# Kernel tuning notes

Hardware: AMD Instinct MI355X
Metric: run time of the kernel (lower is better)

Reference implementation:

```python
import jax, jax.numpy as jnp
import numpy as np

LEVELS = 8
DB2 = [0.4829629131445341, 0.8365163037378079, 0.22414386804185735, -0.12940952255092145]


def make_wavelet(h):
    # g = flip(h); g[1::2] *= -1  (torch compute_wavelet)
    g = jnp.flip(h, -1)
    sign = jnp.where(jnp.arange(g.shape[-1]) % 2 == 0, 1.0, -1.0).astype(g.dtype)
    return g * sign


def circ_conv(x, f, tr=False):
    # FFT-based circular convolution, output length == input length (NORM='backward').
    L = x.shape[-1]
    F = jnp.fft.rfft(f, n=L)
    if tr:
        F = jnp.conj(F)  # circular correlation for the synthesis side
    return jnp.fft.irfft(jnp.fft.rfft(x, n=L) * F, n=L)


def despawn_forward(x, scaling):
    levels = scaling.shape[0]
    L = x.shape[1]
    D = 2 ** int(np.ceil(np.log2(L)))
    pl = (D - L) // 2
    pr = int(np.ceil((D - L) / 2))
    x = jnp.pad(x, ((0, 0), (pl, pr)), mode='edge')  # ReplicationPad1d

    # Analysis: per-level circular filter + dyadic downsample
    approx = x
    details_list = []
    for lev in range(levels):
        h = scaling[lev]
        g = make_wavelet(h)
        d = circ_conv(approx, g)[:, ::2]
        approx = circ_conv(approx, h)[:, ::2]
        details_list.append(d)
    coeffs = details_list + [approx]

    # Synthesis: zero-insert upsample + circular correlation (no thresholding,
    # matching the original forward which never applies HardThreshold)
    rec = approx
    for lev in reversed(range(levels)):
        h = scaling[lev]
        g = make_wavelet(h)
        d = details_list[lev]
        n, m = d.shape
        ud = jnp.zeros((n, 2 * m), d.dtype).at[:, ::2].set(d)
        ua = jnp.zeros((n, 2 * m), rec.dtype).at[:, ::2].set(rec)
        rec = circ_conv(ud, g, tr=True) + circ_conv(ua, h, tr=True)

    return rec[:, pl:L + pr], jnp.concatenate(coeffs, axis=-1)


def setup_inputs() -> dict:
    key = jax.random.key(0)
    k1, _ = jax.random.split(key)
    x = jax.random.normal(k1, (2048, 8192), dtype=jnp.float32)
    scaling = jnp.tile(jnp.asarray(DB2, dtype=jnp.float32), (LEVELS, 1))  # (levels, 4)
    return {"x": x, "scaling": scaling}


def reference(x, scaling):
    return despawn_forward(x, scaling)
```

## Files before the change

kernel.cpp:

```cpp
#include <hip/hip_runtime.h>

#define COLS   8192
#define LEVELS 8
#define TPB    512

__device__ __forceinline__ void bar_lds() {
    asm volatile("s_waitcnt lgkmcnt(0)" ::: "memory");
    __builtin_amdgcn_sched_barrier(0);
    __builtin_amdgcn_s_barrier();
    __builtin_amdgcn_sched_barrier(0);
}

__global__ __launch_bounds__(TPB) void despawn_kernel(
    const float* __restrict__ x, const float* __restrict__ scaling,
    float* __restrict__ out, int rows)
{
    __shared__ __align__(16) float B[COLS / 2];
    __shared__ __align__(16) float C[COLS / 4];
    __shared__ __align__(16) float D[COLS / 4];
    __shared__ float filt[LEVELS * 4];

    const int row = blockIdx.x;
    const int tid = threadIdx.x;

    if (tid < LEVELS * 4) filt[tid] = scaling[tid];
    bar_lds();

    const float* __restrict__ xg       = x + (size_t)row * COLS;
    float* __restrict__       out_rec  = out + (size_t)row * COLS;
    float* __restrict__       out_coef = out + (size_t)rows * COLS + (size_t)row * COLS;

    {
        const float h0 = filt[0], h1 = filt[1], h2 = filt[2], h3 = filt[3];
        const float g0 = h3, g1 = -h2, g2 = h1, g3 = -h0;
        const float4* __restrict__ xg4 = reinterpret_cast<const float4*>(xg);
        const int q8 = COLS / 8, qm = COLS / 4 - 1;
        for (int i = tid; i < q8; i += TPB) {
            const float4 va = xg4[(2 * i - 1) & qm];
            const float4 vb = xg4[2 * i];
            const float4 vc = xg4[2 * i + 1];
            float4 dv, av;
            dv.x = g0*vb.x + g1*va.w + g2*va.z + g3*va.y;
            av.x = h0*vb.x + h1*va.w + h2*va.z + h3*va.y;
            dv.y = g0*vb.z + g1*vb.y + g2*vb.x + g3*va.w;
            av.y = h0*vb.z + h1*vb.y + h2*vb.x + h3*va.w;
            dv.z = g0*vc.x + g1*vb.w + g2*vb.z + g3*vb.y;
            av.z = h0*vc.x + h1*vb.w + h2*vb.z + h3*vb.y;
            dv.w = g0*vc.z + g1*vc.y + g2*vc.x + g3*vb.w;
            av.w = h0*vc.z + h1*vc.y + h2*vc.x + h3*vb.w;
            reinterpret_cast<float4*>(out_coef)[i] = dv;
            reinterpret_cast<float4*>(B)[i]        = av;
        }
        bar_lds();
    }

    int n = COLS / 2, coff = COLS / 2, dOff = 0;
    float* cur = B;
    float* nxt = C;
    for (int lev = 1; lev <= 3; ++lev) {
        const float h0 = filt[4*lev+0], h1 = filt[4*lev+1],
                    h2 = filt[4*lev+2], h3 = filt[4*lev+3];
        const float g0 = h3, g1 = -h2, g2 = h1, g3 = -h0;
        const int half = n >> 1, qq = half >> 2, qm = (n >> 2) - 1;
        const float4* c4 = reinterpret_cast<const float4*>(cur);
        float4* o4 = reinterpret_cast<float4*>(out_coef + coff);
        float4* n4 = reinterpret_cast<float4*>(nxt);
        float4* D4 = reinterpret_cast<float4*>(D + dOff);
        const bool toD = (lev >= 2);
        for (int p = tid; p < qq; p += TPB) {
            const float4 va = c4[(2 * p - 1) & qm];
            const float4 vb = c4[2 * p];
            const float4 vc = c4[2 * p + 1];
            float4 dv, av;
            dv.x = g0*vb.x + g1*va.w + g2*va.z + g3*va.y;
            av.x = h0*vb.x + h1*va.w + h2*va.z + h3*va.y;
            dv.y = g0*vb.z + g1*vb.y + g2*vb.x + g3*va.w;
            av.y = h0*vb.z + h1*vb.y + h2*vb.x + h3*va.w;
            dv.z = g0*vc.x + g1*vb.w + g2*vb.z + g3*vb.y;
            av.z = h0*vc.x + h1*vb.w + h2*vb.z + h3*vb.y;
            dv.w = g0*vc.z + g1*vc.y + g2*vc.x + g3*vb.w;
            av.w = h0*vc.z + h1*vc.y + h2*vc.x + h3*vb.w;
            o4[p] = dv;
            n4[p] = av;
            if (toD) D4[p] = dv;
        }
        bar_lds();
        coff += half;
        if (toD) dOff += half;
        n = half;
        float* t = cur; cur = nxt; nxt = t;
    }

    if (tid < 64) {
        float* acur = C;
        float* anxt = B;
        int nn = 512, coffW = 7680, dW = 1536;
        for (int lev = 4; lev <= 7; ++lev) {
            const float h0 = filt[4*lev+0], h1 = filt[4*lev+1],
                        h2 = filt[4*lev+2], h3 = filt[4*lev+3];
            const float g0 = h3, g1 = -h2, g2 = h1, g3 = -h0;
            const int half = nn >> 1, mask = nn - 1;
            for (int i = tid; i < half; i += 64) {
                const int b = 2 * i;
                const float x0 = acur[b];
                const float x1 = acur[(b - 1) & mask];
                const float x2 = acur[(b - 2) & mask];
                const float x3 = acur[(b - 3) & mask];
                const float d = g0*x0 + g1*x1 + g2*x2 + g3*x3;
                const float a = h0*x0 + h1*x1 + h2*x2 + h3*x3;
                D[dW + i] = d;
                out_coef[coffW + i] = d;
                if (lev == 7) { D[2016 + i] = a; out_coef[8160 + i] = a; }
                else          anxt[i] = a;
            }
            __builtin_amdgcn_wave_barrier();
            coffW += half; dW += half; nn = half;
            float* t = acur; acur = anxt; anxt = t;
        }
        int mS = 32, dS = 1984;
        const float* aprevW = D + 2016;
        for (int lev = 7; lev >= 4; --lev) {
            const float h0 = filt[4*lev+0], h1 = filt[4*lev+1],
                        h2 = filt[4*lev+2], h3 = filt[4*lev+3];
            const float g0 = h3, g1 = -h2, g2 = h1, g3 = -h0;
            const int mm = mS - 1;
            float* recW = (lev & 1) ? B : C;
            for (int j = tid; j < mS; j += 64) {
                const float dj  = D[dS + j];
                const float dj1 = D[dS + ((j + 1) & mm)];
                const float dj2 = D[dS + ((j + 2) & mm)];
                const float aj  = aprevW[j];
                const float aj1 = aprevW[(j + 1) & mm];
                const float aj2 = aprevW[(j + 2) & mm];
                recW[2*j]     = g0*dj  + g2*dj1 + h0*aj  + h2*aj1;
                recW[2*j + 1] = g1*dj1 + g3*dj2 + h1*aj1 + h3*aj2;
            }
            __builtin_amdgcn_wave_barrier();
            aprevW = recW; mS <<= 1; dS -= mS;
        }
    }
    __syncthreads();

#define SYNTH_BODY(d2)                                                        \
    for (int p = tid; p < mp; p += TPB) {                                     \
        const float2 dv0 = (d2)[p];                                           \
        const float2 dv1 = (d2)[(p + 1) & mm];                                \
        const float2 av0 = a2[p];                                             \
        const float2 av1 = a2[(p + 1) & mm];                                  \
        const float r0 = g0*dv0.x + g2*dv0.y + h0*av0.x + h2*av0.y;           \
        const float r1 = g1*dv0.y + g3*dv1.x + h1*av0.y + h3*av1.x;           \
        const float r2 = g0*dv0.y + g2*dv1.x + h0*av0.y + h2*av1.x;           \
        const float r3 = g1*dv1.x + g3*dv1.y + h1*av1.x + h3*av1.y;           \
        const float4 rv = make_float4(r0, r1, r2, r3);                        \
        if (last) reinterpret_cast<float4*>(out_rec)[p] = rv;                 \
        else      reinterpret_cast<float4*>(rec)[p]     = rv;                 \
    }

    const float* aprev = C;
    int m = 512;
    for (int lev = 3; lev >= 0; --lev) {
        const float h0 = filt[4*lev+0], h1 = filt[4*lev+1],
                    h2 = filt[4*lev+2], h3 = filt[4*lev+3];
        const float g0 = h3, g1 = -h2, g2 = h1, g3 = -h0;
        const int mp = m >> 1, mm = mp - 1;
        const float2* a2 = reinterpret_cast<const float2*>(aprev);
        float* rec = (lev & 1) ? B : C;
        const bool last = (lev == 0);
        if (lev >= 2) {
            const float2* dL = reinterpret_cast<const float2*>(D + ((lev == 3) ? 1024 : 0));
            SYNTH_BODY(dL)
        } else {
            const float2* __restrict__ dG =
                reinterpret_cast<const float2*>(out_coef + ((lev == 1) ? 4096 : 0));
            SYNTH_BODY(dG)
        }
        if (lev) bar_lds();
        aprev = rec; m <<= 1;
    }
#undef SYNTH_BODY
}

extern "C" void kernel_launch(void* const* d_in, const int* in_sizes, int n_in,
                              void* d_out, int out_size, void* d_ws, size_t ws_size,
                              hipStream_t stream) {
    const float* x       = (const float*)d_in[0];
    const float* scaling = (const float*)d_in[1];
    float* out           = (float*)d_out;
    const int rows = in_sizes[0] / COLS;
    despawn_kernel<<<rows, TPB, 0, stream>>>(x, scaling, out, rows);
}
```

Baseline: 42.76 us.

## Split fused wavelet kernel into separate analysis and synthesis launches

Splits the single per-row kernel into an analysis kernel and a synthesis kernel. The analysis kernel finishes levels 4-7 and the coarse synthesis with one wave, after the other waves exit early, and parks the level-4 approximation in the output buffer. The synthesis kernel reads the detail coefficients and that intermediate back from global memory to do levels 3-0. The intent is that idle waves no longer wait on the single-wave tail section and that the smaller LDS footprint allows higher occupancy. The cost is a second launch and extra global traffic for the re-read coefficients.

```diff
diff --git a/kernel.cpp b/kernel.cpp
--- a/kernel.cpp
+++ b/kernel.cpp
@@ -1,8 +1,7 @@
 #include <hip/hip_runtime.h>
 
-#define COLS   8192
-#define LEVELS 8
-#define TPB    512
+#define COLS 8192
+#define TPB  512
 
 __device__ __forceinline__ void bar_lds() {
     asm volatile("s_waitcnt lgkmcnt(0)" ::: "memory");
@@ -11,19 +10,17 @@
     __builtin_amdgcn_sched_barrier(0);
 }
 
-__global__ __launch_bounds__(TPB) void despawn_kernel(
+__global__ __launch_bounds__(TPB) void despawn_analysis(
     const float* __restrict__ x, const float* __restrict__ scaling,
     float* __restrict__ out, int rows)
 {
-    __shared__ __align__(16) float B[COLS / 2];
-    __shared__ __align__(16) float C[COLS / 4];
-    __shared__ __align__(16) float D[COLS / 4];
-    __shared__ float filt[LEVELS * 4];
+    __shared__ __align__(16) float LA[4096];
+    __shared__ __align__(16) float LB[2048];
+    __shared__ float filt[32];
 
     const int row = blockIdx.x;
     const int tid = threadIdx.x;
-
-    if (tid < LEVELS * 4) filt[tid] = scaling[tid];
+    if (tid < 32) filt[tid] = scaling[tid];
     bar_lds();
 
     const float* __restrict__ xg       = x + (size_t)row * COLS;
@@ -49,133 +46,217 @@
             dv.w = g0*vc.z + g1*vc.y + g2*vc.x + g3*vb.w;
             av.w = h0*vc.z + h1*vc.y + h2*vc.x + h3*vb.w;
             reinterpret_cast<float4*>(out_coef)[i] = dv;
-            reinterpret_cast<float4*>(B)[i]        = av;
-        }
-        bar_lds();
-    }
-
-    int n = COLS / 2, coff = COLS / 2, dOff = 0;
-    float* cur = B;
-    float* nxt = C;
-    for (int lev = 1; lev <= 3; ++lev) {
-        const float h0 = filt[4*lev+0], h1 = filt[4*lev+1],
-                    h2 = filt[4*lev+2], h3 = filt[4*lev+3];
-        const float g0 = h3, g1 = -h2, g2 = h1, g3 = -h0;
-        const int half = n >> 1, qq = half >> 2, qm = (n >> 2) - 1;
-        const float4* c4 = reinterpret_cast<const float4*>(cur);
-        float4* o4 = reinterpret_cast<float4*>(out_coef + coff);
-        float4* n4 = reinterpret_cast<float4*>(nxt);
-        float4* D4 = reinterpret_cast<float4*>(D + dOff);
-        const bool toD = (lev >= 2);
-        for (int p = tid; p < qq; p += TPB) {
-            const float4 va = c4[(2 * p - 1) & qm];
-            const float4 vb = c4[2 * p];
-            const float4 vc = c4[2 * p + 1];
-            float4 dv, av;
-            dv.x = g0*vb.x + g1*va.w + g2*va.z + g3*va.y;
-            av.x = h0*vb.x + h1*va.w + h2*va.z + h3*va.y;
-            dv.y = g0*vb.z + g1*vb.y + g2*vb.x + g3*va.w;
-            av.y = h0*vb.z + h1*vb.y + h2*vb.x + h3*va.w;
-            dv.z = g0*vc.x + g1*vb.w + g2*vb.z + g3*vb.y;
-            av.z = h0*vc.x + h1*vb.w + h2*vb.z + h3*vb.y;
-            dv.w = g0*vc.z + g1*vc.y + g2*vc.x + g3*vb.w;
-            av.w = h0*vc.z + h1*vc.y + h2*vc.x + h3*vb.w;
-            o4[p] = dv;
-            n4[p] = av;
-            if (toD) D4[p] = dv;
-        }
-        bar_lds();
-        coff += half;
-        if (toD) dOff += half;
-        n = half;
-        float* t = cur; cur = nxt; nxt = t;
-    }
-
-    if (tid < 64) {
-        float* acur = C;
-        float* anxt = B;
-        int nn = 512, coffW = 7680, dW = 1536;
-        for (int lev = 4; lev <= 7; ++lev) {
+            reinterpret_cast<float4*>(LA)[i]       = av;
+        }
+        bar_lds();
+    }
+
+    {
+        int n = 4096, coff = 4096;
+        float* cur = LA;
+        float* nxt = LB;
+        for (int lev = 1; lev <= 3; ++lev) {
             const float h0 = filt[4*lev+0], h1 = filt[4*lev+1],
                         h2 = filt[4*lev+2], h3 = filt[4*lev+3];
             const float g0 = h3, g1 = -h2, g2 = h1, g3 = -h0;
-            const int half = nn >> 1, mask = nn - 1;
-            for (int i = tid; i < half; i += 64) {
-                const int b = 2 * i;
-                const float x0 = acur[b];
-                const float x1 = acur[(b - 1) & mask];
-                const float x2 = acur[(b - 2) & mask];
-                const float x3 = acur[(b - 3) & mask];
-                const float d = g0*x0 + g1*x1 + g2*x2 + g3*x3;
-                const float a = h0*x0 + h1*x1 + h2*x2 + h3*x3;
-                D[dW + i] = d;
-                out_coef[coffW + i] = d;
-                if (lev == 7) { D[2016 + i] = a; out_coef[8160 + i] = a; }
-                else          anxt[i] = a;
+            const int half = n >> 1, qq = half >> 2, qm = (n >> 2) - 1;
+            const float4* c4 = reinterpret_cast<const float4*>(cur);
+            float4* o4 = reinterpret_cast<float4*>(out_coef + coff);
+            float4* n4 = reinterpret_cast<float4*>(nxt);
+            for (int p = tid; p < qq; p += TPB) {
+                const float4 va = c4[(2 * p - 1) & qm];
+                const float4 vb = c4[2 * p];
+                const float4 vc = c4[2 * p + 1];
+                float4 dv, av;
+                dv.x = g0*vb.x + g1*va.w + g2*va.z + g3*va.y;
+                av.x = h0*vb.x + h1*va.w + h2*va.z + h3*va.y;
+                dv.y = g0*vb.z + g1*vb.y + g2*vb.x + g3*va.w;
+                av.y = h0*vb.z + h1*vb.y + h2*vb.x + h3*va.w;
+                dv.z = g0*vc.x + g1*vb.w + g2*vb.z + g3*vb.y;
+                av.z = h0*vc.x + h1*vb.w + h2*vb.z + h3*vb.y;
+                dv.w = g0*vc.z + g1*vc.y + g2*vc.x + g3*vb.w;
+                av.w = h0*vc.z + h1*vc.y + h2*vc.x + h3*vb.w;
+                o4[p] = dv;
+                n4[p] = av;
             }
-            __builtin_amdgcn_wave_barrier();
-            coffW += half; dW += half; nn = half;
-            float* t = acur; acur = anxt; anxt = t;
-        }
-        int mS = 32, dS = 1984;
-        const float* aprevW = D + 2016;
-        for (int lev = 7; lev >= 4; --lev) {
-            const float h0 = filt[4*lev+0], h1 = filt[4*lev+1],
-                        h2 = filt[4*lev+2], h3 = filt[4*lev+3];
-            const float g0 = h3, g1 = -h2, g2 = h1, g3 = -h0;
-            const int mm = mS - 1;
-            float* recW = (lev & 1) ? B : C;
-            for (int j = tid; j < mS; j += 64) {
-                const float dj  = D[dS + j];
-                const float dj1 = D[dS + ((j + 1) & mm)];
-                const float dj2 = D[dS + ((j + 2) & mm)];
-                const float aj  = aprevW[j];
-                const float aj1 = aprevW[(j + 1) & mm];
-                const float aj2 = aprevW[(j + 2) & mm];
-                recW[2*j]     = g0*dj  + g2*dj1 + h0*aj  + h2*aj1;
-                recW[2*j + 1] = g1*dj1 + g3*dj2 + h1*aj1 + h3*aj2;
-            }
-            __builtin_amdgcn_wave_barrier();
-            aprevW = recW; mS <<= 1; dS -= mS;
-        }
-    }
-    __syncthreads();
-
-#define SYNTH_BODY(d2)                                                        \
+            bar_lds();
+            coff += half;
+            n = half;
+            float* t = cur; cur = nxt; nxt = t;
+        }
+    }
+
+    if (tid >= 64) return;
+
+    float* P = LA;
+    float* Q = LA + 512;
+    float* Y = LA + 1024;
+    const int lane = tid;
+
+    {
+        const float h0=filt[16],h1=filt[17],h2=filt[18],h3=filt[19];
+        const float g0=h3,g1=-h2,g2=h1,g3=-h0;
+        for (int i = lane; i < 256; i += 64) {
+            const int b = 2*i;
+            const float x0=LB[b], x1=LB[(b-1)&511], x2=LB[(b-2)&511], x3=LB[(b-3)&511];
+            const float d = g0*x0+g1*x1+g2*x2+g3*x3;
+            Y[i] = d; out_coef[7680+i] = d;
+            P[i] = h0*x0+h1*x1+h2*x2+h3*x3;
+        }
+        __builtin_amdgcn_wave_barrier();
+    }
+    {
+        const float h0=filt[20],h1=filt[21],h2=filt[22],h3=filt[23];
+        const float g0=h3,g1=-h2,g2=h1,g3=-h0;
+        for (int i = lane; i < 128; i += 64) {
+            const int b = 2*i;
+            const float x0=P[b], x1=P[(b-1)&255], x2=P[(b-2)&255], x3=P[(b-3)&255];
+            const float d = g0*x0+g1*x1+g2*x2+g3*x3;
+            Y[256+i] = d; out_coef[7936+i] = d;
+            Q[i] = h0*x0+h1*x1+h2*x2+h3*x3;
+        }
+        __builtin_amdgcn_wave_barrier();
+    }
+    {
+        const float h0=filt[24],h1=filt[25],h2=filt[26],h3=filt[27];
+        const float g0=h3,g1=-h2,g2=h1,g3=-h0;
+        if (lane < 64) {
+            const int i = lane, b = 2*i;
+            const float x0=Q[b], x1=Q[(b-1)&127], x2=Q[(b-2)&127], x3=Q[(b-3)&127];
+            const float d = g0*x0+g1*x1+g2*x2+g3*x3;
+            Y[384+i] = d; out_coef[8064+i] = d;
+            P[i] = h0*x0+h1*x1+h2*x2+h3*x3;
+        }
+        __builtin_amdgcn_wave_barrier();
+    }
+    {
+        const float h0=filt[28],h1=filt[29],h2=filt[30],h3=filt[31];
+        const float g0=h3,g1=-h2,g2=h1,g3=-h0;
+        if (lane < 32) {
+            const int i = lane, b = 2*i;
+            const float x0=P[b], x1=P[(b-1)&63], x2=P[(b-2)&63], x3=P[(b-3)&63];
+            const float d = g0*x0+g1*x1+g2*x2+g3*x3;
+            const float a = h0*x0+h1*x1+h2*x2+h3*x3;
+            Y[448+i] = d; out_coef[8128+i] = d;
+            Y[480+i] = a; out_coef[8160+i] = a;
+        }
+        __builtin_amdgcn_wave_barrier();
+    }
+    {
+        const float h0=filt[28],h1=filt[29],h2=filt[30],h3=filt[31];
+        const float g0=h3,g1=-h2,g2=h1,g3=-h0;
+        if (lane < 32) {
+            const int j = lane;
+            const float dj=Y[448+j], dj1=Y[448+((j+1)&31)], dj2=Y[448+((j+2)&31)];
+            const float aj=Y[480+j], aj1=Y[480+((j+1)&31)], aj2=Y[480+((j+2)&31)];
+            Q[2*j]   = g0*dj  + g2*dj1 + h0*aj  + h2*aj1;
+            Q[2*j+1] = g1*dj1 + g3*dj2 + h1*aj1 + h3*aj2;
+        }
+        __builtin_amdgcn_wave_barrier();
+    }
+    {
+        const float h0=filt[24],h1=filt[25],h2=filt[26],h3=filt[27];
+        const float g0=h3,g1=-h2,g2=h1,g3=-h0;
+        if (lane < 64) {
+            const int j = lane;
+            const float dj=Y[384+j], dj1=Y[384+((j+1)&63)], dj2=Y[384+((j+2)&63)];
+            const float aj=Q[j], aj1=Q[(j+1)&63], aj2=Q[(j+2)&63];
+            P[2*j]   = g0*dj  + g2*dj1 + h0*aj  + h2*aj1;
+            P[2*j+1] = g1*dj1 + g3*dj2 + h1*aj1 + h3*aj2;
+        }
+        __builtin_amdgcn_wave_barrier();
+    }
+    {
+        const float h0=filt[20],h1=filt[21],h2=filt[22],h3=filt[23];
+        const float g0=h3,g1=-h2,g2=h1,g3=-h0;
+        for (int j = lane; j < 128; j += 64) {
+            const float dj=Y[256+j], dj1=Y[256+((j+1)&127)], dj2=Y[256+((j+2)&127)];
+            const float aj=P[j], aj1=P[(j+1)&127], aj2=P[(j+2)&127];
+            Q[2*j]   = g0*dj  + g2*dj1 + h0*aj  + h2*aj1;
+            Q[2*j+1] = g1*dj1 + g3*dj2 + h1*aj1 + h3*aj2;
+        }
+        __builtin_amdgcn_wave_barrier();
+    }
+    {
+        const float h0=filt[16],h1=filt[17],h2=filt[18],h3=filt[19];
+        const float g0=h3,g1=-h2,g2=h1,g3=-h0;
+        float2* __restrict__ st = reinterpret_cast<float2*>(out_rec + 512);
+        for (int j = lane; j < 256; j += 64) {
+            const float dj=Y[j], dj1=Y[(j+1)&255], dj2=Y[(j+2)&255];
+            const float aj=Q[j], aj1=Q[(j+1)&255], aj2=Q[(j+2)&255];
+            const float r0 = g0*dj  + g2*dj1 + h0*aj  + h2*aj1;
+            const float r1 = g1*dj1 + g3*dj2 + h1*aj1 + h3*aj2;
+            st[j] = make_float2(r0, r1);
+        }
+    }
+}
+
+__global__ __launch_bounds__(TPB) void despawn_synth(
+    const float* __restrict__ scaling, float* __restrict__ out, int rows)
+{
+    __shared__ __align__(16) float LA[4096];
+    __shared__ __align__(16) float LB[4096];
+    __shared__ float filt[32];
+
+    const int row = blockIdx.x;
+    const int tid = threadIdx.x;
+    if (tid < 32) filt[tid] = scaling[tid];
+    bar_lds();
+
+    float* __restrict__       out_rec  = out + (size_t)row * COLS;
+    const float* __restrict__ out_coef = out + (size_t)rows * COLS + (size_t)row * COLS;
+
+#define SYNTH_BODY(d2, a2, dst4, toG)                                         \
     for (int p = tid; p < mp; p += TPB) {                                     \
         const float2 dv0 = (d2)[p];                                           \
         const float2 dv1 = (d2)[(p + 1) & mm];                                \
-        const float2 av0 = a2[p];                                             \
-        const float2 av1 = a2[(p + 1) & mm];                                  \
+        const float2 av0 = (a2)[p];                                           \
+        const float2 av1 = (a2)[(p + 1) & mm];                                \
         const float r0 = g0*dv0.x + g2*dv0.y + h0*av0.x + h2*av0.y;           \
         const float r1 = g1*dv0.y + g3*dv1.x + h1*av0.y + h3*av1.x;           \
         const float r2 = g0*dv0.y + g2*dv1.x + h0*av0.y + h2*av1.x;           \
         const float r3 = g1*dv1.x + g3*dv1.y + h1*av1.x + h3*av1.y;           \
-        const float4 rv = make_float4(r0, r1, r2, r3);                        \
-        if (last) reinterpret_cast<float4*>(out_rec)[p] = rv;                 \
-        else      reinterpret_cast<float4*>(rec)[p]     = rv;                 \
-    }
-
-    const float* aprev = C;
-    int m = 512;
-    for (int lev = 3; lev >= 0; --lev) {
-        const float h0 = filt[4*lev+0], h1 = filt[4*lev+1],
-                    h2 = filt[4*lev+2], h3 = filt[4*lev+3];
-        const float g0 = h3, g1 = -h2, g2 = h1, g3 = -h0;
-        const int mp = m >> 1, mm = mp - 1;
-        const float2* a2 = reinterpret_cast<const float2*>(aprev);
-        float* rec = (lev & 1) ? B : C;
-        const bool last = (lev == 0);
-        if (lev >= 2) {
-            const float2* dL = reinterpret_cast<const float2*>(D + ((lev == 3) ? 1024 : 0));
-            SYNTH_BODY(dL)
-        } else {
-            const float2* __restrict__ dG =
-                reinterpret_cast<const float2*>(out_coef + ((lev == 1) ? 4096 : 0));
-            SYNTH_BODY(dG)
-        }
-        if (lev) bar_lds();
-        aprev = rec; m <<= 1;
+        (dst4)[p] = make_float4(r0, r1, r2, r3);                              \
+    }
+
+    {
+        const float h0=filt[12],h1=filt[13],h2=filt[14],h3=filt[15];
+        const float g0=h3,g1=-h2,g2=h1,g3=-h0;
+        const int mp = 256, mm = 255;
+        const float2* __restrict__ d2 = reinterpret_cast<const float2*>(out_coef + 7168);
+        const float2* __restrict__ a2 = reinterpret_cast<const float2*>(out_rec + 512);
+        float4* dst4 = reinterpret_cast<float4*>(LB);
+        SYNTH_BODY(d2, a2, dst4, false)
+        bar_lds();
+    }
+    {
+        const float h0=filt[8],h1=filt[9],h2=filt[10],h3=filt[11];
+        const float g0=h3,g1=-h2,g2=h1,g3=-h0;
+        const int mp = 512, mm = 511;
+        const float2* __restrict__ d2 = reinterpret_cast<const float2*>(out_coef + 6144);
+        const float2* a2 = reinterpret_cast<const float2*>(LB);
+        float4* dst4 = reinterpret_cast<float4*>(LA);
+        SYNTH_BODY(d2, a2, dst4, false)
+        bar_lds();
+    }
+    {
+        const float h0=filt[4],h1=filt[5],h2=filt[6],h3=filt[7];
+        const float g0=h3,g1=-h2,g2=h1,g3=-h0;
+        const int mp = 1024, mm = 1023;
+        const float2* __restrict__ d2 = reinterpret_cast<const float2*>(out_coef + 4096);
+        const float2* a2 = reinterpret_cast<const float2*>(LA);
+        float4* dst4 = reinterpret_cast<float4*>(LB);
+        SYNTH_BODY(d2, a2, dst4, false)
+        bar_lds();
+    }
+    {
+        const float h0=filt[0],h1=filt[1],h2=filt[2],h3=filt[3];
+        const float g0=h3,g1=-h2,g2=h1,g3=-h0;
+        const int mp = 2048, mm = 2047;
+        const float2* __restrict__ d2 = reinterpret_cast<const float2*>(out_coef);
+        const float2* a2 = reinterpret_cast<const float2*>(LB);
+        float4* __restrict__ dst4 = reinterpret_cast<float4*>(out_rec);
+        SYNTH_BODY(d2, a2, dst4, true)
     }
 #undef SYNTH_BODY
 }
@@ -187,5 +268,6 @@
     const float* scaling = (const float*)d_in[1];
     float* out           = (float*)d_out;
     const int rows = in_sizes[0] / COLS;
-    despawn_kernel<<<rows, TPB, 0, stream>>>(x, scaling, out, rows);
-}
+    despawn_analysis<<<rows, TPB, 0, stream>>>(x, scaling, out, rows);
+    despawn_synth<<<rows, TPB, 0, stream>>>(scaling, out, rows);
+}
```

Result: slower. 48.39 us (+13.1%).

## Replace single-wave tail and barriered synthesis with register/shuffle per-wave pipeline

Applied to the files above, without the earlier changes.

Every wave now redundantly computes analysis levels 4-7 and synthesis levels 7-4 in registers using cross-lane shuffles, instead of one wave working through LDS while the other waves wait. Synthesis levels 3-0 are then computed per wave from registers, with halo values recomputed locally. This removes the block-wide barriers between those levels. Filters are read directly from global memory rather than staged in LDS. The cost is duplicated arithmetic and higher register pressure, plus fragile index logic at the boundaries.

```diff
diff --git a/kernel.cpp b/kernel.cpp
--- a/kernel.cpp
+++ b/kernel.cpp
@@ -1,8 +1,7 @@
 #include <hip/hip_runtime.h>
 
-#define COLS   8192
-#define LEVELS 8
-#define TPB    512
+#define COLS 8192
+#define TPB  512
 
 __device__ __forceinline__ void bar_lds() {
     asm volatile("s_waitcnt lgkmcnt(0)" ::: "memory");
@@ -10,28 +9,65 @@
     __builtin_amdgcn_s_barrier();
     __builtin_amdgcn_sched_barrier(0);
 }
+__device__ __forceinline__ void wait_lds() {
+    asm volatile("s_waitcnt lgkmcnt(0)" ::: "memory");
+    __builtin_amdgcn_sched_barrier(0);
+}
+
+#define ANA_LEVEL(CIN, ain, aout, dout, F0, F1, F2, F3)                       \
+    {                                                                         \
+        const int _src = (l - 1) & 63;                                        \
+        const float _m1 = __shfl(ain[(CIN)-1], _src);                         \
+        const float _m2 = __shfl(ain[(CIN)-2], _src);                         \
+        const float _m3 = __shfl(ain[(CIN)-3], _src);                         \
+        dout[0] = (F3)*ain[0] - (F2)*_m1 + (F1)*_m2 - (F0)*_m3;               \
+        aout[0] = (F0)*ain[0] + (F1)*_m1 + (F2)*_m2 + (F3)*_m3;               \
+        dout[1] = (F3)*ain[2] - (F2)*ain[1] + (F1)*ain[0] - (F0)*_m1;         \
+        aout[1] = (F0)*ain[2] + (F1)*ain[1] + (F2)*ain[0] + (F3)*_m1;         \
+        _Pragma("unroll")                                                     \
+        for (int _j = 2; _j < (CIN)/2; ++_j) {                                \
+            dout[_j] = (F3)*ain[2*_j] - (F2)*ain[2*_j-1] + (F1)*ain[2*_j-2] - (F0)*ain[2*_j-3]; \
+            aout[_j] = (F0)*ain[2*_j] + (F1)*ain[2*_j-1] + (F2)*ain[2*_j-2] + (F3)*ain[2*_j-3]; \
+        }                                                                     \
+    }
+
+#define SYN_LEVEL(CD, din, ain, rout, F0, F1, F2, F3)                         \
+    {                                                                         \
+        const int _src = (l + 1) & 63;                                        \
+        const float _d0 = __shfl(din[0], _src);                               \
+        const float _d1 = __shfl(din[1], _src);                               \
+        const float _a0 = __shfl(ain[0], _src);                               \
+        const float _a1 = __shfl(ain[1], _src);                               \
+        _Pragma("unroll")                                                     \
+        for (int _j = 0; _j < (CD); ++_j) {                                   \
+            const float dj  = din[_j];                                        \
+            const float dj1 = (_j+1 < (CD)) ? din[_j+1] : _d0;                \
+            const float dj2 = (_j+2 < (CD)) ? din[_j+2] : ((_j+1 < (CD)) ? _d0 : _d1); \
+            const float aj  = ain[_j];                                        \
+            const float aj1 = (_j+1 < (CD)) ? ain[_j+1] : _a0;                \
+            const float aj2 = (_j+2 < (CD)) ? ain[_j+2] : ((_j+1 < (CD)) ? _a0 : _a1); \
+            rout[2*_j]   = (F3)*dj + (F1)*dj1 + (F0)*aj + (F2)*aj1;           \
+            rout[2*_j+1] = -(F2)*dj1 - (F0)*dj2 + (F1)*aj1 + (F3)*aj2;        \
+        }                                                                     \
+    }
 
 __global__ __launch_bounds__(TPB) void despawn_kernel(
     const float* __restrict__ x, const float* __restrict__ scaling,
     float* __restrict__ out, int rows)
 {
-    __shared__ __align__(16) float B[COLS / 2];
-    __shared__ __align__(16) float C[COLS / 4];
-    __shared__ __align__(16) float D[COLS / 4];
-    __shared__ float filt[LEVELS * 4];
+    __shared__ __align__(16) float B[4096];
+    __shared__ __align__(16) float C[2048];
+    __shared__ __align__(16) float D[1536];
 
     const int row = blockIdx.x;
     const int tid = threadIdx.x;
-
-    if (tid < LEVELS * 4) filt[tid] = scaling[tid];
-    bar_lds();
 
     const float* __restrict__ xg       = x + (size_t)row * COLS;
     float* __restrict__       out_rec  = out + (size_t)row * COLS;
     float* __restrict__       out_coef = out + (size_t)rows * COLS + (size_t)row * COLS;
 
     {
-        const float h0 = filt[0], h1 = filt[1], h2 = filt[2], h3 = filt[3];
+        const float h0 = scaling[0], h1 = scaling[1], h2 = scaling[2], h3 = scaling[3];
         const float g0 = h3, g1 = -h2, g2 = h1, g3 = -h0;
         const float4* __restrict__ xg4 = reinterpret_cast<const float4*>(xg);
         const int q8 = COLS / 8, qm = COLS / 4 - 1;
@@ -54,130 +90,219 @@
         bar_lds();
     }
 
-    int n = COLS / 2, coff = COLS / 2, dOff = 0;
-    float* cur = B;
-    float* nxt = C;
-    for (int lev = 1; lev <= 3; ++lev) {
-        const float h0 = filt[4*lev+0], h1 = filt[4*lev+1],
-                    h2 = filt[4*lev+2], h3 = filt[4*lev+3];
-        const float g0 = h3, g1 = -h2, g2 = h1, g3 = -h0;
-        const int half = n >> 1, qq = half >> 2, qm = (n >> 2) - 1;
-        const float4* c4 = reinterpret_cast<const float4*>(cur);
-        float4* o4 = reinterpret_cast<float4*>(out_coef + coff);
-        float4* n4 = reinterpret_cast<float4*>(nxt);
-        float4* D4 = reinterpret_cast<float4*>(D + dOff);
-        const bool toD = (lev >= 2);
-        for (int p = tid; p < qq; p += TPB) {
-            const float4 va = c4[(2 * p - 1) & qm];
-            const float4 vb = c4[2 * p];
-            const float4 vc = c4[2 * p + 1];
-            float4 dv, av;
-            dv.x = g0*vb.x + g1*va.w + g2*va.z + g3*va.y;
-            av.x = h0*vb.x + h1*va.w + h2*va.z + h3*va.y;
-            dv.y = g0*vb.z + g1*vb.y + g2*vb.x + g3*va.w;
-            av.y = h0*vb.z + h1*vb.y + h2*vb.x + h3*va.w;
-            dv.z = g0*vc.x + g1*vb.w + g2*vb.z + g3*vb.y;
-            av.z = h0*vc.x + h1*vb.w + h2*vb.z + h3*vb.y;
-            dv.w = g0*vc.z + g1*vc.y + g2*vc.x + g3*vb.w;
-            av.w = h0*vc.z + h1*vc.y + h2*vc.x + h3*vb.w;
-            o4[p] = dv;
-            n4[p] = av;
-            if (toD) D4[p] = dv;
-        }
-        bar_lds();
-        coff += half;
-        if (toD) dOff += half;
-        n = half;
-        float* t = cur; cur = nxt; nxt = t;
-    }
-
-    if (tid < 64) {
-        float* acur = C;
-        float* anxt = B;
-        int nn = 512, coffW = 7680, dW = 1536;
-        for (int lev = 4; lev <= 7; ++lev) {
-            const float h0 = filt[4*lev+0], h1 = filt[4*lev+1],
-                        h2 = filt[4*lev+2], h3 = filt[4*lev+3];
+    {
+        int n = COLS / 2, coff = COLS / 2, dOff = 0;
+        float* cur = B;
+        float* nxt = C;
+        for (int lev = 1; lev <= 3; ++lev) {
+            const float h0 = scaling[4*lev+0], h1 = scaling[4*lev+1],
+                        h2 = scaling[4*lev+2], h3 = scaling[4*lev+3];
             const float g0 = h3, g1 = -h2, g2 = h1, g3 = -h0;
-            const int half = nn >> 1, mask = nn - 1;
-            for (int i = tid; i < half; i += 64) {
-                const int b = 2 * i;
-                const float x0 = acur[b];
-                const float x1 = acur[(b - 1) & mask];
-                const float x2 = acur[(b - 2) & mask];
-                const float x3 = acur[(b - 3) & mask];
-                const float d = g0*x0 + g1*x1 + g2*x2 + g3*x3;
-                const float a = h0*x0 + h1*x1 + h2*x2 + h3*x3;
-                D[dW + i] = d;
-                out_coef[coffW + i] = d;
-                if (lev == 7) { D[2016 + i] = a; out_coef[8160 + i] = a; }
-                else          anxt[i] = a;
+            const int half = n >> 1, qq = half >> 2, qm = (n >> 2) - 1;
+            const float4* c4 = reinterpret_cast<const float4*>(cur);
+            float4* o4 = reinterpret_cast<float4*>(out_coef + coff);
+            float4* n4 = reinterpret_cast<float4*>(nxt);
+            float4* D4 = reinterpret_cast<float4*>(D + dOff);
+            const bool toD = (lev >= 2);
+            for (int p = tid; p < qq; p += TPB) {
+                const float4 va = c4[(2 * p - 1) & qm];
+                const float4 vb = c4[2 * p];
+                const float4 vc = c4[2 * p + 1];
+                float4 dv, av;
+                dv.x = g0*vb.x + g1*va.w + g2*va.z + g3*va.y;
+                av.x = h0*vb.x + h1*va.w + h2*va.z + h3*va.y;
+                dv.y = g0*vb.z + g1*vb.y + g2*vb.x + g3*va.w;
+                av.y = h0*vb.z + h1*vb.y + h2*vb.x + h3*va.w;
+                dv.z = g0*vc.x + g1*vb.w + g2*vb.z + g3*vb.y;
+                av.z = h0*vc.x + h1*vb.w + h2*vb.z + h3*vb.y;
+                dv.w = g0*vc.z + g1*vc.y + g2*vc.x + g3*vb.w;
+                av.w = h0*vc.z + h1*vc.y + h2*vc.x + h3*vb.w;
+                o4[p] = dv;
+                n4[p] = av;
+                if (toD) D4[p] = dv;
             }
-            __builtin_amdgcn_wave_barrier();
-            coffW += half; dW += half; nn = half;
-            float* t = acur; acur = anxt; anxt = t;
-        }
-        int mS = 32, dS = 1984;
-        const float* aprevW = D + 2016;
-        for (int lev = 7; lev >= 4; --lev) {
-            const float h0 = filt[4*lev+0], h1 = filt[4*lev+1],
-                        h2 = filt[4*lev+2], h3 = filt[4*lev+3];
-            const float g0 = h3, g1 = -h2, g2 = h1, g3 = -h0;
-            const int mm = mS - 1;
-            float* recW = (lev & 1) ? B : C;
-            for (int j = tid; j < mS; j += 64) {
-                const float dj  = D[dS + j];
-                const float dj1 = D[dS + ((j + 1) & mm)];
-                const float dj2 = D[dS + ((j + 2) & mm)];
-                const float aj  = aprevW[j];
-                const float aj1 = aprevW[(j + 1) & mm];
-                const float aj2 = aprevW[(j + 2) & mm];
-                recW[2*j]     = g0*dj  + g2*dj1 + h0*aj  + h2*aj1;
-                recW[2*j + 1] = g1*dj1 + g3*dj2 + h1*aj1 + h3*aj2;
-            }
-            __builtin_amdgcn_wave_barrier();
-            aprevW = recW; mS <<= 1; dS -= mS;
-        }
-    }
-    __syncthreads();
-
-#define SYNTH_BODY(d2)                                                        \
-    for (int p = tid; p < mp; p += TPB) {                                     \
-        const float2 dv0 = (d2)[p];                                           \
-        const float2 dv1 = (d2)[(p + 1) & mm];                                \
-        const float2 av0 = a2[p];                                             \
-        const float2 av1 = a2[(p + 1) & mm];                                  \
-        const float r0 = g0*dv0.x + g2*dv0.y + h0*av0.x + h2*av0.y;           \
-        const float r1 = g1*dv0.y + g3*dv1.x + h1*av0.y + h3*av1.x;           \
-        const float r2 = g0*dv0.y + g2*dv1.x + h0*av0.y + h2*av1.x;           \
-        const float r3 = g1*dv1.x + g3*dv1.y + h1*av1.x + h3*av1.y;           \
-        const float4 rv = make_float4(r0, r1, r2, r3);                        \
-        if (last) reinterpret_cast<float4*>(out_rec)[p] = rv;                 \
-        else      reinterpret_cast<float4*>(rec)[p]     = rv;                 \
-    }
-
-    const float* aprev = C;
-    int m = 512;
-    for (int lev = 3; lev >= 0; --lev) {
-        const float h0 = filt[4*lev+0], h1 = filt[4*lev+1],
-                    h2 = filt[4*lev+2], h3 = filt[4*lev+3];
-        const float g0 = h3, g1 = -h2, g2 = h1, g3 = -h0;
-        const int mp = m >> 1, mm = mp - 1;
-        const float2* a2 = reinterpret_cast<const float2*>(aprev);
-        float* rec = (lev & 1) ? B : C;
-        const bool last = (lev == 0);
-        if (lev >= 2) {
-            const float2* dL = reinterpret_cast<const float2*>(D + ((lev == 3) ? 1024 : 0));
-            SYNTH_BODY(dL)
-        } else {
-            const float2* __restrict__ dG =
-                reinterpret_cast<const float2*>(out_coef + ((lev == 1) ? 4096 : 0));
-            SYNTH_BODY(dG)
-        }
-        if (lev) bar_lds();
-        aprev = rec; m <<= 1;
-    }
-#undef SYNTH_BODY
+            if (lev == 3) __syncthreads();
+            else          bar_lds();
+            coff += half;
+            if (toD) dOff += half;
+            n = half;
+            float* t = cur; cur = nxt; nxt = t;
+        }
+    }
+
+    const int w = tid >> 6;
+    const int l = tid & 63;
+
+    float a3r[8];
+    {
+        const float4 v0 = reinterpret_cast<const float4*>(C)[2*l];
+        const float4 v1 = reinterpret_cast<const float4*>(C)[2*l+1];
+        a3r[0]=v0.x; a3r[1]=v0.y; a3r[2]=v0.z; a3r[3]=v0.w;
+        a3r[4]=v1.x; a3r[5]=v1.y; a3r[6]=v1.z; a3r[7]=v1.w;
+    }
+    float a4r[4], d4r[4];
+    ANA_LEVEL(8, a3r, a4r, d4r, scaling[16], scaling[17], scaling[18], scaling[19]);
+    float a5r[2], d5r[2];
+    ANA_LEVEL(4, a4r, a5r, d5r, scaling[20], scaling[21], scaling[22], scaling[23]);
+    float a6r, d6r;
+    {
+        const float F0=scaling[24],F1=scaling[25],F2=scaling[26],F3=scaling[27];
+        const int s1 = (l-1)&63, s2 = (l-2)&63;
+        const float x0 = a5r[0];
+        const float x1 = __shfl(a5r[1], s1);
+        const float x2 = __shfl(a5r[0], s1);
+        const float x3 = __shfl(a5r[1], s2);
+        d6r = F3*x0 - F2*x1 + F1*x2 - F0*x3;
+        a6r = F0*x0 + F1*x1 + F2*x2 + F3*x3;
+    }
+    float d7r, apr;
+    {
+        const float F0=scaling[28],F1=scaling[29],F2=scaling[30],F3=scaling[31];
+        const int i2 = 2*l;
+        const float x0 = __shfl(a6r, i2 & 63);
+        const float x1 = __shfl(a6r, (i2-1)&63);
+        const float x2 = __shfl(a6r, (i2-2)&63);
+        const float x3 = __shfl(a6r, (i2-3)&63);
+        d7r = F3*x0 - F2*x1 + F1*x2 - F0*x3;
+        apr = F0*x0 + F1*x1 + F2*x2 + F3*x3;
+    }
+    if (w == 0) {
+        reinterpret_cast<float4*>(out_coef + 7680)[l] = make_float4(d4r[0],d4r[1],d4r[2],d4r[3]);
+        reinterpret_cast<float2*>(out_coef + 7936)[l] = make_float2(d5r[0],d5r[1]);
+        out_coef[8064 + l] = d6r;
+        if (l < 32) { out_coef[8128 + l] = d7r; out_coef[8160 + l] = apr; }
+    }
+    float rec7;
+    {
+        const float F0=scaling[28],F1=scaling[29],F2=scaling[30],F3=scaling[31];
+        const float dj = d7r, dj1 = __shfl(d7r,(l+1)&31), dj2 = __shfl(d7r,(l+2)&31);
+        const float aj = apr, aj1 = __shfl(apr,(l+1)&31), aj2 = __shfl(apr,(l+2)&31);
+        const float r0 = F3*dj + F1*dj1 + F0*aj + F2*aj1;
+        const float r1 = -F2*dj1 - F0*dj2 + F1*aj1 + F3*aj2;
+        const float e0 = __shfl(r0, l>>1);
+        const float e1 = __shfl(r1, l>>1);
+        rec7 = (l & 1) ? e1 : e0;
+    }
+    float rec6[2];
+    {
+        const float F0=scaling[24],F1=scaling[25],F2=scaling[26],F3=scaling[27];
+        const float dj = d6r, dj1 = __shfl(d6r,(l+1)&63), dj2 = __shfl(d6r,(l+2)&63);
+        const float aj = rec7, aj1 = __shfl(rec7,(l+1)&63), aj2 = __shfl(rec7,(l+2)&63);
+        rec6[0] = F3*dj + F1*dj1 + F0*aj + F2*aj1;
+        rec6[1] = -F2*dj1 - F0*dj2 + F1*aj1 + F3*aj2;
+    }
+    float rec5[4];
+    SYN_LEVEL(2, d5r, rec6, rec5, scaling[20], scaling[21], scaling[22], scaling[23]);
+    float rec4r[8];
+    SYN_LEVEL(4, d4r, rec5, rec4r, scaling[16], scaling[17], scaling[18], scaling[19]);
+    reinterpret_cast<float4*>(C + 512)[2*l]   = make_float4(rec4r[0],rec4r[1],rec4r[2],rec4r[3]);
+    reinterpret_cast<float4*>(C + 512)[2*l+1] = make_float4(rec4r[4],rec4r[5],rec4r[6],rec4r[7]);
+    wait_lds();
+
+    float rec3[2], r3h[4];
+    {
+        const float F0=scaling[12],F1=scaling[13],F2=scaling[14],F3=scaling[15];
+        const int j = 64*w + l;
+        const float a0v = C[512 + (j & 511)];
+        const float a1v = C[512 + ((j+1) & 511)];
+        const float a2v = C[512 + ((j+2) & 511)];
+        const float e0  = D[1024 + (j & 511)];
+        const float e1  = D[1024 + ((j+1) & 511)];
+        const float e2  = D[1024 + ((j+2) & 511)];
+        rec3[0] = F3*e0 + F1*e1 + F0*a0v + F2*a1v;
+        rec3[1] = -F2*e1 - F0*e2 + F1*a1v + F3*a2v;
+        #pragma unroll
+        for (int q = 0; q < 2; ++q) {
+            const int jh = 64*(w+1) + q;
+            const float A0 = C[512 + (jh & 511)];
+            const float A1 = C[512 + ((jh+1) & 511)];
+            const float A2 = C[512 + ((jh+2) & 511)];
+            const float E0 = D[1024 + (jh & 511)];
+            const float E1 = D[1024 + ((jh+1) & 511)];
+            const float E2 = D[1024 + ((jh+2) & 511)];
+            r3h[2*q]   = F3*E0 + F1*E1 + F0*A0 + F2*A1;
+            r3h[2*q+1] = -F2*E1 - F0*E2 + F1*A1 + F3*A2;
+        }
+    }
+    float rec2[4], r2h[3];
+    {
+        const float F0=scaling[8],F1=scaling[9],F2=scaling[10],F3=scaling[11];
+        const int lp1 = (l+1)&63;
+        const float n0 = __shfl(rec3[0], lp1);
+        const float n1 = __shfl(rec3[1], lp1);
+        const float b2 = (l==63) ? r3h[0] : n0;
+        const float b3 = (l==63) ? r3h[1] : n1;
+        const int jj = 128*w + 2*l;
+        const float e0 = D[jj & 1023], e1 = D[(jj+1)&1023],
+                    e2 = D[(jj+2)&1023], e3 = D[(jj+3)&1023];
+        rec2[0] = F3*e0 + F1*e1 + F0*rec3[0] + F2*rec3[1];
+        rec2[1] = -F2*e1 - F0*e2 + F1*rec3[1] + F3*b2;
+        rec2[2] = F3*e1 + F1*e2 + F0*rec3[1] + F2*b2;
+        rec2[3] = -F2*e2 - F0*e3 + F1*b2 + F3*b3;
+        const int jh = 128*(w+1);
+        const float E0 = D[jh & 1023], E1 = D[(jh+1)&1023], E2 = D[(jh+2)&1023];
+        r2h[0] = F3*E0 + F1*E1 + F0*r3h[0] + F2*r3h[1];
+        r2h[1] = -F2*E1 - F0*E2 + F1*r3h[1] + F3*r3h[2];
+        r2h[2] = F3*E1 + F1*E2 + F0*r3h[1] + F2*r3h[2];
+    }
+    float rec1[8], r1h[2];
+    {
+        const float F0=scaling[4],F1=scaling[5],F2=scaling[6],F3=scaling[7];
+        const float* __restrict__ d1g = out_coef + 4096;
+        const int jb = 256*w + 4*l;
+        float dw[6];
+        {
+            const float4 v = *reinterpret_cast<const float4*>(d1g + jb);
+            dw[0]=v.x; dw[1]=v.y; dw[2]=v.z; dw[3]=v.w;
+            const float2 v2 = *reinterpret_cast<const float2*>(d1g + ((jb+4)&2047));
+            dw[4]=v2.x; dw[5]=v2.y;
+        }
+        const int lp1 = (l+1)&63;
+        const float n0 = __shfl(rec2[0], lp1);
+        const float n1 = __shfl(rec2[1], lp1);
+        const float A4 = (l==63) ? r2h[0] : n0;
+        const float A5 = (l==63) ? r2h[1] : n1;
+        const float A[6] = {rec2[0],rec2[1],rec2[2],rec2[3],A4,A5};
+        #pragma unroll
+        for (int p = 0; p < 4; ++p) {
+            rec1[2*p]   = F3*dw[p] + F1*dw[p+1] + F0*A[p] + F2*A[p+1];
+            rec1[2*p+1] = -F2*dw[p+1] - F0*dw[p+2] + F1*A[p+1] + F3*A[p+2];
+        }
+        const int jh = (256*(w+1)) & 2047;
+        const float H0 = d1g[jh], H1 = d1g[(jh+1)&2047], H2 = d1g[(jh+2)&2047];
+        r1h[0] = F3*H0 + F1*H1 + F0*r2h[0] + F2*r2h[1];
+        r1h[1] = -F2*H1 - F0*H2 + F1*r2h[1] + F3*r2h[2];
+    }
+    {
+        const float F0=scaling[0],F1=scaling[1],F2=scaling[2],F3=scaling[3];
+        const float* __restrict__ d0g = out_coef;
+        const int jb = 512*w + 8*l;
+        float dw[10];
+        {
+            const float4 v0 = *reinterpret_cast<const float4*>(d0g + jb);
+            const float4 v1 = *reinterpret_cast<const float4*>(d0g + jb + 4);
+            const float2 v2 = *reinterpret_cast<const float2*>(d0g + ((jb+8)&4095));
+            dw[0]=v0.x; dw[1]=v0.y; dw[2]=v0.z; dw[3]=v0.w;
+            dw[4]=v1.x; dw[5]=v1.y; dw[6]=v1.z; dw[7]=v1.w;
+            dw[8]=v2.x; dw[9]=v2.y;
+        }
+        const int lp1 = (l+1)&63;
+        const float n0 = __shfl(rec1[0], lp1);
+        const float n1 = __shfl(rec1[1], lp1);
+        const float A8 = (l==63) ? r1h[0] : n0;
+        const float A9 = (l==63) ? r1h[1] : n1;
+        const float A[10] = {rec1[0],rec1[1],rec1[2],rec1[3],rec1[4],rec1[5],rec1[6],rec1[7],A8,A9};
+        float4* __restrict__ o4 = reinterpret_cast<float4*>(out_rec + 1024*w + 16*l);
+        #pragma unroll
+        for (int c = 0; c < 4; ++c) {
+            float4 rv;
+            rv.x = F3*dw[2*c]   + F1*dw[2*c+1] + F0*A[2*c]   + F2*A[2*c+1];
+            rv.y = -F2*dw[2*c+1] - F0*dw[2*c+2] + F1*A[2*c+1] + F3*A[2*c+2];
+            rv.z = F3*dw[2*c+1] + F1*dw[2*c+2] + F0*A[2*c+1] + F2*A[2*c+2];
+            rv.w = -F2*dw[2*c+2] - F0*dw[2*c+3] + F1*A[2*c+2] + F3*A[2*c+3];
+            o4[c] = rv;
+        }
+    }
 }
 
 extern "C" void kernel_launch(void* const* d_in, const int* in_sizes, int n_in,
```

After: 46.04 us. +7.7%, slower.
